# Performance work log

Measured on AMD Instinct MI355X. Metric: run time of the kernel, lower is better.

The kernel has to match this reference:

```python
import jax, jax.numpy as jnp
import numpy as np

D = 1024
H = 16
HD = D // H
T = 2048
B = 2
HID = 4 * D
EPS = 1e-5


def setup_inputs() -> dict:
    key = jax.random.key(0)
    ks = jax.random.split(key, 8)
    s = lambda fan_in: 1.0 / np.sqrt(fan_in)
    return {
        "x": jax.random.normal(ks[0], (B, T, D), dtype=jnp.float32),
        "ln1_g": jnp.ones((D,), jnp.float32),
        "ln1_b": jnp.zeros((D,), jnp.float32),
        "Wqkv": jax.random.uniform(ks[1], (D, 3 * D), jnp.float32, -s(D), s(D)),
        "bqkv": jnp.zeros((3 * D,), jnp.float32),
        "Wout": jax.random.uniform(ks[2], (D, D), jnp.float32, -s(D), s(D)),
        "bout": jnp.zeros((D,), jnp.float32),
        "ln2_g": jnp.ones((D,), jnp.float32),
        "ln2_b": jnp.zeros((D,), jnp.float32),
        "W1": jax.random.uniform(ks[3], (D, HID), jnp.float32, -s(D), s(D)),
        "b1": jnp.zeros((HID,), jnp.float32),
        "W2": jax.random.uniform(ks[4], (HID, D), jnp.float32, -s(HID), s(HID)),
        "b2": jnp.zeros((D,), jnp.float32),
    }


def _layernorm(h, g, b):
    mu = jnp.mean(h, axis=-1, keepdims=True)
    var = jnp.mean(jnp.square(h - mu), axis=-1, keepdims=True)
    return (h - mu) * jax.lax.rsqrt(var + EPS) * g + b


def reference(x, ln1_g, ln1_b, Wqkv, bqkv, Wout, bout, ln2_g, ln2_b, W1, b1, W2, b2):
    b, t, d = x.shape
    scale = 1.0 / np.sqrt(HD)

    # --- attention (pre-LN) ---
    h = _layernorm(x, ln1_g, ln1_b)
    qkv = h @ Wqkv + bqkv                      # [b, t, 3d]
    q, k, v = jnp.split(qkv, 3, axis=-1)
    q = q.reshape(b, t, H, HD)
    k = k.reshape(b, t, H, HD)
    v = v.reshape(b, t, H, HD)
    scores = jnp.einsum("bqhd,bkhd->bhqk", q, k) * scale  # [b, h, t, t]
    causal = jnp.tril(jnp.ones((t, t), dtype=bool))
    scores = jnp.where(causal, scores, -jnp.inf)
    attn = jax.nn.softmax(scores, axis=-1)
    out = jnp.einsum("bhqk,bkhd->bqhd", attn, v).reshape(b, t, d)
    x = x + (out @ Wout + bout)

    # --- MLP (pre-LN) ---
    h = _layernorm(x, ln2_g, ln2_b)
    h = jax.nn.gelu(h @ W1 + b1, approximate=False)
    x = x + (h @ W2 + b2)
    return x
```

## Files before the change

kernel.cpp:

```cpp
#include <hip/hip_runtime.h>
#include <hip/hip_bf16.h>
#include <math.h>

#define DD 1024
#define TT 2048
#define BB 2
#define HH 16
#define HDIM 64
#define HIDD 4096

typedef __attribute__((ext_vector_type(4))) float f32x4;
typedef __attribute__((ext_vector_type(8))) __bf16 bf16x8;
typedef __attribute__((ext_vector_type(4))) __bf16 bf16x4;

#define MF16 __builtin_amdgcn_mfma_f32_16x16x32_bf16

__device__ __forceinline__ void gload_lds16(const void* g, void* l) {
  __builtin_amdgcn_global_load_lds(
      (const __attribute__((address_space(1))) void*)g,
      (__attribute__((address_space(3))) void*)l, 16, 0, 0);
}

__global__ __launch_bounds__(256) void castT64(const float* __restrict__ W,
                                               __bf16* __restrict__ Wt,
                                               int K, int N) {
  __shared__ float t[64][65];
  const int n0 = blockIdx.x * 64, k0 = blockIdx.y * 64;
#pragma unroll
  for (int e = 0; e < 16; ++e) {
    int idx = e * 256 + threadIdx.x;
    int rr = idx >> 6, cc = idx & 63;
    t[rr][cc] = W[(size_t)(k0 + rr) * N + n0 + cc];
  }
  __syncthreads();
#pragma unroll
  for (int e = 0; e < 16; ++e) {
    int idx = e * 256 + threadIdx.x;
    int rr = idx >> 6, cc = idx & 63;
    Wt[(size_t)(n0 + rr) * K + k0 + cc] = (__bf16)t[cc][rr];
  }
}

__global__ __launch_bounds__(256) void ln_fwd(const float* __restrict__ x,
                                              const float* __restrict__ gamma,
                                              const float* __restrict__ beta,
                                              __bf16* __restrict__ out) {
  const int row = blockIdx.x;
  const int t4 = threadIdx.x;
  const float4 v = reinterpret_cast<const float4*>(x + (size_t)row * DD)[t4];
  float s = v.x + v.y + v.z + v.w;
  float ss = v.x * v.x + v.y * v.y + v.z * v.z + v.w * v.w;
#pragma unroll
  for (int m = 32; m >= 1; m >>= 1) { s += __shfl_xor(s, m); ss += __shfl_xor(ss, m); }
  __shared__ float red[8];
  const int wave = threadIdx.x >> 6, lane = threadIdx.x & 63;
  if (lane == 0) { red[wave] = s; red[4 + wave] = ss; }
  __syncthreads();
  s = red[0] + red[1] + red[2] + red[3];
  ss = red[4] + red[5] + red[6] + red[7];
  const float mu = s * (1.0f / DD);
  const float rs = rsqrtf(ss * (1.0f / DD) - mu * mu + 1e-5f);
  const float4 gm = reinterpret_cast<const float4*>(gamma)[t4];
  const float4 bt = reinterpret_cast<const float4*>(beta)[t4];
  bf16x4 o;
  o[0] = (__bf16)((v.x - mu) * rs * gm.x + bt.x);
  o[1] = (__bf16)((v.y - mu) * rs * gm.y + bt.y);
  o[2] = (__bf16)((v.z - mu) * rs * gm.z + bt.z);
  o[3] = (__bf16)((v.w - mu) * rs * gm.w + bt.w);
  *reinterpret_cast<bf16x4*>(out + (size_t)row * DD + t4 * 4) = o;
}

template <int MODE>
__global__ __launch_bounds__(512, 1) void gemm8(const __bf16* __restrict__ A,
                                                const __bf16* __restrict__ Bt,
                                                const float* __restrict__ bias,
                                                void* __restrict__ out0,
                                                __bf16* __restrict__ q1,
                                                __bf16* __restrict__ q2,
                                                __bf16* __restrict__ q3,
                                                int N, int K, int kchunk) {
  const int tid = threadIdx.x;
  const int wid = tid >> 6, lane = tid & 63;
  const int g = lane >> 4, r = lane & 15;
  const int wrh = wid >> 2;
  const int wc = (wid & 3) * 64;

  int bm, bn, kbase, zz;
  if constexpr (MODE == 3) {
    const int L = blockIdx.x;
    const int xcd = L & 7, idx = L >> 3;
    zz = xcd >> 1;
    bm = (((xcd & 1) << 3) + (idx >> 2)) * 256;
    bn = (idx & 3) * 256;
    kbase = zz * kchunk;
  } else {
    const int gx = gridDim.x;
    const int nwg = gx * gridDim.y;
    const int orig = blockIdx.y * gx + blockIdx.x;
    const int swz = (orig & 7) * (nwg >> 3) + (orig >> 3);
    const int bn4 = swz & 3;
    const int bmt = (swz >> 2) % gx;
    const int bng = (swz >> 2) / gx;
    bm = bmt * 256;
    bn = (bng * 4 + bn4) * 256;
    kbase = 0;
    zz = 0;
  }

  const int NT = kchunk >> 6;
  const __bf16* Asrc = A + (size_t)bm * K + kbase;
  const __bf16* Bsrc = Bt + (size_t)bn * K + kbase;

  __shared__ __bf16 lds[2][4][8192];

  f32x4 acc[8][4] = {};
  bf16x8 bfr[4][2];

  auto STG = [&](int ab, int h, int kt) {
    const __bf16* src = (ab ? Bsrc : Asrc) + (size_t)h * 128 * K;
    char* dst = (char*)&lds[kt & 1][ab * 2 + h][0];
#pragma unroll
    for (int gl = 0; gl < 2; ++gl) {
      const int o = gl * 8192 + wid * 1024 + lane * 16;
      const int row = o >> 7;
      const int cbs = (o & 127) ^ (((row >> 2) & 1) << 5);
      gload_lds16((const char*)src + (size_t)row * (K * 2) + kt * 128 + cbs,
                  dst + gl * 8192 + wid * 1024);
    }
  };
  auto DSA = [&](int s, int mi, int kk) -> bf16x8 {
    return *(const bf16x8*)((const char*)&lds[s][wrh][0] + (mi * 16 + r) * 128 +
                            ((kk * 64 + g * 16) ^ ((r & 4) << 3)));
  };
  auto DSB = [&](int s, int nj, int kk) -> bf16x8 {
    const int rt = wc + nj * 16 + r;
    return *(const bf16x8*)((const char*)&lds[s][2 + (rt >> 7)][0] + (rt & 127) * 128 +
                            ((kk * 64 + g * 16) ^ ((r & 4) << 3)));
  };

#define PH(S, Q, STAGE_STMT, WAIT_STMT)                                        \
  {                                                                            \
    if (Q == 0) {                                                              \
      _Pragma("unroll") for (int nj = 0; nj < 4; ++nj) {                       \
        bfr[nj][0] = DSB(S, nj, 0);                                            \
        bfr[nj][1] = DSB(S, nj, 1);                                            \
      }                                                                        \
    }                                                                          \
    bf16x8 a00 = DSA(S, 2 * Q, 0), a01 = DSA(S, 2 * Q, 1);                     \
    bf16x8 a10 = DSA(S, 2 * Q + 1, 0), a11 = DSA(S, 2 * Q + 1, 1);             \
    STAGE_STMT;                                                                \
    WAIT_STMT;                                                                 \
    __builtin_amdgcn_s_barrier();                                              \
    asm volatile("s_waitcnt lgkmcnt(0)" ::: "memory");                         \
    __builtin_amdgcn_s_setprio(1);                                             \
    _Pragma("unroll") for (int nj = 0; nj < 4; ++nj) {                         \
      acc[2 * Q][nj] = MF16(a00, bfr[nj][0], acc[2 * Q][nj], 0, 0, 0);         \
      acc[2 * Q][nj] = MF16(a01, bfr[nj][1], acc[2 * Q][nj], 0, 0, 0);         \
      acc[2 * Q + 1][nj] = MF16(a10, bfr[nj][0], acc[2 * Q + 1][nj], 0, 0, 0); \
      acc[2 * Q + 1][nj] = MF16(a11, bfr[nj][1], acc[2 * Q + 1][nj], 0, 0, 0); \
    }                                                                          \
    __builtin_amdgcn_s_setprio(0);                                             \
    __builtin_amdgcn_s_barrier();                                              \
  }

  STG(1, 0, 0); STG(1, 1, 0); STG(0, 0, 0); STG(0, 1, 0);
  STG(1, 0, 1); STG(1, 1, 1); STG(0, 0, 1);
  asm volatile("s_waitcnt vmcnt(6)" ::: "memory");
  __builtin_amdgcn_s_barrier();

  const int NI = NT >> 1;
  for (int i = 0; i < NI; ++i) {
    const int k2 = 2 * i + 2, k3 = 2 * i + 3;
    const bool nl = (i + 1 < NI);
    PH(0, 0, { STG(0, 1, 2 * i + 1); }, {});
    PH(0, 1, { if (nl) STG(1, 0, k2); }, {});
    PH(0, 2, { if (nl) STG(1, 1, k2); }, {});
    PH(0, 3, { if (nl) STG(0, 0, k2); },
       { if (nl) asm volatile("s_waitcnt vmcnt(6)" ::: "memory");
         else    asm volatile("s_waitcnt vmcnt(0)" ::: "memory"); });
    PH(1, 0, { if (nl) STG(0, 1, k2); }, {});
    PH(1, 1, { if (nl) STG(1, 0, k3); }, {});
    PH(1, 2, { if (nl) STG(1, 1, k3); }, {});
    PH(1, 3, { if (nl) STG(0, 0, k3); },
       { if (nl) asm volatile("s_waitcnt vmcnt(6)" ::: "memory"); });
  }
#undef PH

  const int row0 = bm + wrh * 128 + g * 4;
  const int col0 = bn + wc + r;
#pragma unroll
  for (int mi = 0; mi < 8; ++mi) {
#pragma unroll
    for (int nj = 0; nj < 4; ++nj) {
      const int col = col0 + nj * 16;
      float bv = 0.0f;
      if constexpr (MODE != 3) bv = bias[col];
#pragma unroll
      for (int i4 = 0; i4 < 4; ++i4) {
        const int rowg = row0 + mi * 16 + i4;
        const size_t idx = (size_t)rowg * N + col;
        const float v = acc[mi][nj][i4];
        if constexpr (MODE == 0) {
          if (bn >= 2048) {
            const int cv = col - 2048;
            const int hv = cv >> 6, dv = cv & 63;
            const int bq = rowg >> 11, tq = rowg & 2047;
            q1[(((size_t)bq * 16 + hv) * 64 + dv) * 2048 + tq] = (__bf16)(v + bv);
          } else {
            ((__bf16*)out0)[idx] = (__bf16)(v + bv);
          }
        } else if constexpr (MODE == 2) {
          const float t = v + bv;
          const float u2 = t * (1.5957691216f + t * t * 0.0713548163f);
          ((__bf16*)out0)[idx] = (__bf16)(t * __builtin_amdgcn_rcpf(1.0f + __expf(-u2)));
        } else {
          if (zz == 0) {
            ((float*)out0)[idx] = v;
          } else {
            __bf16* p = (zz == 1 ? q1 : (zz == 2 ? q2 : q3));
            p[idx] = (__bf16)v;
          }
        }
      }
    }
  }
}

__global__ __launch_bounds__(256) void reduceW2(const __bf16* __restrict__ p1,
                                                const __bf16* __restrict__ p2,
                                                const __bf16* __restrict__ p3,
                                                const float* __restrict__ x1,
                                                const float* __restrict__ b2,
                                                float* __restrict__ out) {
  const size_t i8 = ((size_t)blockIdx.x * 256 + threadIdx.x) * 8;
  const int col0 = (int)(i8 & 1023);
  bf16x8 a = *(const bf16x8*)(p1 + i8);
  bf16x8 b = *(const bf16x8*)(p2 + i8);
  bf16x8 c = *(const bf16x8*)(p3 + i8);
  float4 o0 = *(const float4*)(out + i8);
  float4 o1 = *(const float4*)(out + i8 + 4);
  const float4 xv0 = *(const float4*)(x1 + i8);
  const float4 xv1 = *(const float4*)(x1 + i8 + 4);
  const float4 bb0 = *(const float4*)(b2 + col0);
  const float4 bb1 = *(const float4*)(b2 + col0 + 4);
  float* op0 = (float*)&o0;
  float* op1 = (float*)&o1;
  const float* xp0 = (const float*)&xv0;
  const float* xp1 = (const float*)&xv1;
  const float* bp0 = (const float*)&bb0;
  const float* bp1 = (const float*)&bb1;
#pragma unroll
  for (int j = 0; j < 4; ++j)
    op0[j] += xp0[j] + bp0[j] + (float)a[j] + (float)b[j] + (float)c[j];
#pragma unroll
  for (int j = 0; j < 4; ++j)
    op1[j] += xp1[j] + bp1[j] + (float)a[4 + j] + (float)b[4 + j] + (float)c[4 + j];
  *(float4*)(out + i8) = o0;
  *(float4*)(out + i8 + 4) = o1;
}

template <int MODE>
__global__ __launch_bounds__(256) void gemm_bt(const __bf16* __restrict__ A,
                                               const __bf16* __restrict__ Bt,
                                               const float* __restrict__ bias,
                                               const float* __restrict__ resid,
                                               void* __restrict__ Cout,
                                               int M, int N, int K) {
  __shared__ __bf16 As[128 * 32];
  __shared__ __bf16 Bs[128 * 32];
  const int tid = threadIdx.x;
  const int wave = tid >> 6, lane = tid & 63;
  const int g = lane >> 4, r = lane & 15;
  const int gx = gridDim.x;
  const int nwg = gx * gridDim.y;
  const int orig = blockIdx.y * gx + blockIdx.x;
  const int swz = (orig & 7) * (nwg >> 3) + (orig >> 3);
  const int bn4 = swz & 3;
  const int bmt = (swz >> 2) % gx;
  const int bng = (swz >> 2) / gx;
  const int bm = bmt * 128;
  const int bn = (bng * 4 + bn4) * 128;
  const int wr = (wave >> 1) * 64, wc = (wave & 1) * 64;
  f32x4 acc[4][4] = {};

  const int off0 = wave * 2048 + lane * 16;
  const int off1 = off0 + 1024;
  const int sr0 = off0 >> 6, sk0 = (off0 & 63) >> 1;
  const int sr1 = off1 >> 6, sk1 = (off1 & 63) >> 1;
  const __bf16* gA0 = A + (size_t)(bm + sr0) * K + sk0;
  const __bf16* gA1 = A + (size_t)(bm + sr1) * K + sk1;
  const __bf16* gB0 = Bt + (size_t)(bn + sr0) * K + sk0;
  const __bf16* gB1 = Bt + (size_t)(bn + sr1) * K + sk1;
  char* lA0 = (char*)As + wave * 2048;
  char* lA1 = lA0 + 1024;
  char* lB0 = (char*)Bs + wave * 2048;
  char* lB1 = lB0 + 1024;

  for (int k0 = 0; k0 < K; k0 += 32) {
    gload_lds16(gA0 + k0, lA0);
    gload_lds16(gA1 + k0, lA1);
    gload_lds16(gB0 + k0, lB0);
    gload_lds16(gB1 + k0, lB1);
    __syncthreads();
    bf16x8 af[4], bf[4];
#pragma unroll
    for (int mi = 0; mi < 4; ++mi)
      af[mi] = *reinterpret_cast<const bf16x8*>(&As[(wr + mi * 16 + r) * 32 + g * 8]);
#pragma unroll
    for (int ni = 0; ni < 4; ++ni)
      bf[ni] = *reinterpret_cast<const bf16x8*>(&Bs[(wc + ni * 16 + r) * 32 + g * 8]);
    __builtin_amdgcn_s_setprio(1);
#pragma unroll
    for (int mi = 0; mi < 4; ++mi)
#pragma unroll
      for (int ni = 0; ni < 4; ++ni)
        acc[mi][ni] = MF16(af[mi], bf[ni], acc[mi][ni], 0, 0, 0);
    __builtin_amdgcn_s_setprio(0);
    __syncthreads();
  }

  const int row0 = bm + wr + 4 * g;
  const int col0 = bn + wc + r;
#pragma unroll
  for (int mi = 0; mi < 4; ++mi) {
#pragma unroll
    for (int ni = 0; ni < 4; ++ni) {
      const int col = col0 + ni * 16;
      const float bv = bias[col];
#pragma unroll
      for (int i = 0; i < 4; ++i) {
        const int row = row0 + mi * 16 + i;
        const size_t idx = (size_t)row * N + col;
        float v = acc[mi][ni][i] + bv;
        if (MODE == 0) {
          ((__bf16*)Cout)[idx] = (__bf16)v;
        } else if (MODE == 1) {
          ((float*)Cout)[idx] = v + resid[idx];
        } else {
          const float u2 = v * (1.5957691216f + v * v * 0.0713548163f);
          const float gl = v * __builtin_amdgcn_rcpf(1.0f + __expf(-u2));
          ((__bf16*)Cout)[idx] = (__bf16)gl;
        }
      }
    }
  }
}

__device__ __forceinline__ void stage_kv(const __bf16* __restrict__ src_row0, int rstride,
                                         int wave, int lane, char* tile) {
#pragma unroll
  for (int qq = 0; qq < 2; ++qq) {
    const int o = wave * 2048 + qq * 1024 + lane * 16;
    const int p = o >> 12, row = (o >> 6) & 63, cb = (o >> 4) & 3;
    gload_lds16(src_row0 + (size_t)row * rstride + p * 32 + cb * 8,
                tile + wave * 2048 + qq * 1024);
  }
}

__global__ __launch_bounds__(256) void attn_fwd(const __bf16* __restrict__ qkv,
                                                const __bf16* __restrict__ vtg,
                                                __bf16* __restrict__ atto) {
  const int orig = blockIdx.y * gridDim.x + blockIdx.x;
  const int swz = (orig & 7) * 64 + (orig >> 3);
  const int bh = swz >> 4;
  const int j = swz & 15;
  const int b = bh >> 4, h = bh & 15;
  const int tid = threadIdx.x;
  const int wave = tid >> 6, lane = tid & 63;
  const int g = lane >> 4, r = lane & 15;

  __shared__ __bf16 Qs[2 * 64 * 32];
  __shared__ __bf16 Ks[2][2 * 64 * 32];
  __shared__ __bf16 Vs[2][2 * 64 * 32];
  __shared__ __bf16 Pl[4][2 * 16 * 32];

  const __bf16* ksrc = qkv + (size_t)(b * TT) * 3072 + 1024 + h * 64;
  const __bf16* vsrc = vtg + (size_t)bh * 64 * 2048;
  const float C2 = 0.18033688011112042f;

  for (int ph = 0; ph < 2; ++ph) {
    const int qt = ph ? (31 - j) : j;
    const int q0 = qt * 64;
    stage_kv(qkv + (size_t)(b * TT + q0) * 3072 + h * 64, 3072, wave, lane, (char*)Qs);
    stage_kv(ksrc, 3072, wave, lane, (char*)Ks[0]);
    stage_kv(vsrc, 2048, wave, lane, (char*)Vs[0]);

    f32x4 oacc[4] = {};
    float m_s[4], l_s[4];
#pragma unroll
    for (int i = 0; i < 4; ++i) { m_s[i] = -1e30f; l_s[i] = 0.0f; }

    const int nt = qt + 1;
    int cur = 0;
    for (int t = 0; t < nt; ++t) {
      const int kv0 = t * 64;
      __syncthreads();
      if (t + 1 < nt) {
        stage_kv(ksrc + (size_t)(kv0 + 64) * 3072, 3072, wave, lane, (char*)Ks[cur ^ 1]);
        stage_kv(vsrc + kv0 + 64, 2048, wave, lane, (char*)Vs[cur ^ 1]);
      }
      bf16x8 qf[2];
#pragma unroll
      for (int kp = 0; kp < 2; ++kp)
        qf[kp] = *reinterpret_cast<const bf16x8*>(&Qs[kp * 2048 + (wave * 16 + r) * 32 + g * 8]);
      f32x4 s[4];
#pragma unroll
      for (int cn = 0; cn < 4; ++cn) s[cn] = f32x4{0.f, 0.f, 0.f, 0.f};
      __builtin_amdgcn_s_setprio(1);
#pragma unroll
      for (int cn = 0; cn < 4; ++cn)
#pragma unroll
        for (int kp = 0; kp < 2; ++kp) {
          bf16x8 bk = *reinterpret_cast<const bf16x8*>(
              &Ks[cur][kp * 2048 + (cn * 16 + r) * 32 + g * 8]);
          s[cn] = MF16(qf[kp], bk, s[cn], 0, 0, 0);
        }
      __builtin_amdgcn_s_setprio(0);
      const int rowg = q0 + wave * 16 + 4 * g;
      float pm[4];
#pragma unroll
      for (int i = 0; i < 4; ++i) pm[i] = -1e30f;
#pragma unroll
      for (int cn = 0; cn < 4; ++cn) {
        const int colg = kv0 + cn * 16 + r;
#pragma unroll
        for (int i = 0; i < 4; ++i) {
          float v = s[cn][i] * C2;
          v = (colg > rowg + i) ? -1e30f : v;
          s[cn][i] = v;
          pm[i] = fmaxf(pm[i], v);
        }
      }
      const int upd = __any((pm[0] > m_s[0] + 8.0f) || (pm[1] > m_s[1] + 8.0f) ||
                            (pm[2] > m_s[2] + 8.0f) || (pm[3] > m_s[3] + 8.0f));
      if (upd) {
#pragma unroll
        for (int i = 0; i < 4; ++i) {
          pm[i] = fmaxf(pm[i], __shfl_xor(pm[i], 1));
          pm[i] = fmaxf(pm[i], __shfl_xor(pm[i], 2));
          pm[i] = fmaxf(pm[i], __shfl_xor(pm[i], 4));
          pm[i] = fmaxf(pm[i], __shfl_xor(pm[i], 8));
          const float mn = fmaxf(m_s[i], pm[i]);
          const float sf = __builtin_amdgcn_exp2f(m_s[i] - mn);
          m_s[i] = mn;
          l_s[i] *= sf;
#pragma unroll
          for (int ni = 0; ni < 4; ++ni) oacc[ni][i] *= sf;
        }
      }
      float psum[4] = {0.f, 0.f, 0.f, 0.f};
#pragma unroll
      for (int cn = 0; cn < 4; ++cn)
#pragma unroll
        for (int i = 0; i < 4; ++i) {
          const float p = __builtin_amdgcn_exp2f(s[cn][i] - m_s[i]);
          s[cn][i] = p;
          psum[i] += p;
        }
#pragma unroll
      for (int i = 0; i < 4; ++i) {
        psum[i] += __shfl_xor(psum[i], 1);
        psum[i] += __shfl_xor(psum[i], 2);
        psum[i] += __shfl_xor(psum[i], 4);
        psum[i] += __shfl_xor(psum[i], 8);
        l_s[i] += psum[i];
      }
#pragma unroll
      for (int cn = 0; cn < 4; ++cn)
#pragma unroll
        for (int i = 0; i < 4; ++i)
          Pl[wave][(cn >> 1) * 512 + (4 * g + i) * 32 + (cn & 1) * 16 + r] = (__bf16)s[cn][i];
      bf16x8 pa[2];
#pragma unroll
      for (int kp = 0; kp < 2; ++kp)
        pa[kp] = *reinterpret_cast<const bf16x8*>(&Pl[wave][kp * 512 + r * 32 + g * 8]);
      __builtin_amdgcn_s_setprio(1);
#pragma unroll
      for (int ni = 0; ni < 4; ++ni)
#pragma unroll
        for (int kp = 0; kp < 2; ++kp) {
          bf16x8 bv = *reinterpret_cast<const bf16x8*>(
              &Vs[cur][kp * 2048 + (ni * 16 + r) * 32 + g * 8]);
          oacc[ni] = MF16(pa[kp], bv, oacc[ni], 0, 0, 0);
        }
      __builtin_amdgcn_s_setprio(0);
      cur ^= 1;
    }

#pragma unroll
    for (int i = 0; i < 4; ++i) {
      const float inv = 1.0f / l_s[i];
      const size_t rowo = (size_t)(b * TT + q0 + wave * 16 + 4 * g + i) * DD + h * 64;
#pragma unroll
      for (int ni = 0; ni < 4; ++ni)
        atto[rowo + ni * 16 + r] = (__bf16)(oacc[ni][i] * inv);
    }
    __syncthreads();
  }
}

extern "C" void kernel_launch(void* const* d_in, const int* in_sizes, int n_in,
                              void* d_out, int out_size, void* d_ws, size_t ws_size,
                              hipStream_t stream) {
  const float* x     = (const float*)d_in[0];
  const float* ln1_g = (const float*)d_in[1];
  const float* ln1_b = (const float*)d_in[2];
  const float* Wqkv  = (const float*)d_in[3];
  const float* bqkv  = (const float*)d_in[4];
  const float* Wout  = (const float*)d_in[5];
  const float* bout  = (const float*)d_in[6];
  const float* ln2_g = (const float*)d_in[7];
  const float* ln2_b = (const float*)d_in[8];
  const float* W1    = (const float*)d_in[9];
  const float* b1    = (const float*)d_in[10];
  const float* W2    = (const float*)d_in[11];
  const float* b2    = (const float*)d_in[12];
  float* out = (float*)d_out;

  char* ws = (char*)d_ws;
  const size_t MB = 1024 * 1024;
  __bf16* WqkvT = (__bf16*)(ws);
  __bf16* WoutT = (__bf16*)(ws + 6 * MB);
  __bf16* W1T   = (__bf16*)(ws + 8 * MB);
  __bf16* W2T   = (__bf16*)(ws + 16 * MB);
  float*  x1    = (float*)(ws + 24 * MB);
  __bf16* vtg   = (__bf16*)(ws + 24 * MB);
  __bf16* hbuf  = (__bf16*)(ws + 40 * MB);
  __bf16* qkvb  = (__bf16*)(ws + 48 * MB);
  __bf16* atto  = (__bf16*)(ws + 72 * MB);
  __bf16* mlp1  = (__bf16*)(ws + 48 * MB);
  __bf16* p1b   = (__bf16*)(ws);
  __bf16* p2b   = (__bf16*)(ws + 8 * MB);
  __bf16* p3b   = (__bf16*)(ws + 40 * MB);

  castT64<<<dim3(48, 16), 256, 0, stream>>>(Wqkv, WqkvT, 1024, 3072);
  castT64<<<dim3(16, 16), 256, 0, stream>>>(Wout, WoutT, 1024, 1024);
  castT64<<<dim3(64, 16), 256, 0, stream>>>(W1, W1T, 1024, 4096);
  castT64<<<dim3(16, 64), 256, 0, stream>>>(W2, W2T, 4096, 1024);

  ln_fwd<<<4096, 256, 0, stream>>>(x, ln1_g, ln1_b, hbuf);
  gemm8<0><<<dim3(16, 12), 512, 0, stream>>>(hbuf, WqkvT, bqkv, qkvb, vtg, nullptr, nullptr,
                                             3072, 1024, 1024);
  attn_fwd<<<dim3(16, 32), 256, 0, stream>>>(qkvb, vtg, atto);
  gemm_bt<1><<<dim3(32, 8), 256, 0, stream>>>(atto, WoutT, bout, x, x1, 4096, 1024, 1024);

  ln_fwd<<<4096, 256, 0, stream>>>(x1, ln2_g, ln2_b, hbuf);
  gemm8<2><<<dim3(16, 16), 512, 0, stream>>>(hbuf, W1T, b1, mlp1, nullptr, nullptr, nullptr,
                                             4096, 1024, 1024);
  gemm8<3><<<dim3(256, 1), 512, 0, stream>>>(mlp1, W2T, nullptr, out, p1b, p2b, p3b,
                                             1024, 4096, 1024);
  reduceW2<<<2048, 256, 0, stream>>>(p1b, p2b, p3b, x1, b2, out);
}
```

Baseline: 270.4 us.

## Move V transpose to a dedicated kernel and streamline attention softmax inner loop

The QKV GEMM epilogue no longer writes V transposed with scattered strided stores. A separate LDS-based transpose kernel now produces the V^T buffer with coalesced vector loads and stores. In attention, causal masking is skipped for tiles fully below the diagonal, and the per-iteration row-sum shuffle reduction is deferred to one reduction at the end. The P staging buffer in LDS also gets an XOR swizzle to reduce bank conflicts. The cost is an extra kernel launch and an additional read and write of V.

```diff
diff --git a/kernel.cpp b/kernel.cpp
--- a/kernel.cpp
+++ b/kernel.cpp
@@ -201,14 +201,7 @@
         const size_t idx = (size_t)rowg * N + col;
         const float v = acc[mi][nj][i4];
         if constexpr (MODE == 0) {
-          if (bn >= 2048) {
-            const int cv = col - 2048;
-            const int hv = cv >> 6, dv = cv & 63;
-            const int bq = rowg >> 11, tq = rowg & 2047;
-            q1[(((size_t)bq * 16 + hv) * 64 + dv) * 2048 + tq] = (__bf16)(v + bv);
-          } else {
-            ((__bf16*)out0)[idx] = (__bf16)(v + bv);
-          }
+          ((__bf16*)out0)[idx] = (__bf16)(v + bv);
         } else if constexpr (MODE == 2) {
           const float t = v + bv;
           const float u2 = t * (1.5957691216f + t * t * 0.0713548163f);
@@ -346,6 +339,37 @@
   }
 }
 
+__global__ __launch_bounds__(256) void vtrans(const __bf16* __restrict__ qkv,
+                                              __bf16* __restrict__ vtg) {
+  const int bh = blockIdx.y, b = bh >> 4, h = bh & 15;
+  const int t0 = blockIdx.x * 64;
+  const int tid = threadIdx.x, wave = tid >> 6, lane = tid & 63;
+  __shared__ __bf16 tile[64 * 64];
+#pragma unroll
+  for (int e = 0; e < 2; ++e) {
+    const int gid = e * 256 + tid;
+    const int row = gid >> 3, d0 = (gid & 7) * 8;
+    bf16x8 v = *reinterpret_cast<const bf16x8*>(
+        qkv + (size_t)(b * TT + t0 + row) * 3072 + 2048 + h * 64 + d0);
+    const int slot = (d0 >> 3) ^ (row & 7);
+    *reinterpret_cast<bf16x8*>((char*)tile + row * 128 + slot * 16) = v;
+  }
+  __syncthreads();
+  const int d = lane;
+#pragma unroll
+  for (int e = 0; e < 2; ++e) {
+    const int k0 = (wave * 2 + e) * 8;
+    bf16x8 o;
+#pragma unroll
+    for (int j = 0; j < 8; ++j) {
+      const int row = k0 + j;
+      o[j] = *(const __bf16*)((const char*)tile + row * 128 +
+                              (((d >> 3) ^ (row & 7)) << 4) + (d & 7) * 2);
+    }
+    *reinterpret_cast<bf16x8*>(&vtg[((size_t)bh * 64 + d) * 2048 + t0 + k0]) = o;
+  }
+}
+
 __device__ __forceinline__ void stage_kv(const __bf16* __restrict__ src_row0, int rstride,
                                          int wave, int lane, char* tile) {
 #pragma unroll
@@ -420,16 +444,27 @@
       float pm[4];
 #pragma unroll
       for (int i = 0; i < 4; ++i) pm[i] = -1e30f;
-#pragma unroll
-      for (int cn = 0; cn < 4; ++cn) {
-        const int colg = kv0 + cn * 16 + r;
-#pragma unroll
-        for (int i = 0; i < 4; ++i) {
-          float v = s[cn][i] * C2;
-          v = (colg > rowg + i) ? -1e30f : v;
-          s[cn][i] = v;
-          pm[i] = fmaxf(pm[i], v);
-        }
+      if (kv0 + 63 > q0 + wave * 16) {
+#pragma unroll
+        for (int cn = 0; cn < 4; ++cn) {
+          const int colg = kv0 + cn * 16 + r;
+#pragma unroll
+          for (int i = 0; i < 4; ++i) {
+            float v = s[cn][i] * C2;
+            v = (colg > rowg + i) ? -1e30f : v;
+            s[cn][i] = v;
+            pm[i] = fmaxf(pm[i], v);
+          }
+        }
+      } else {
+#pragma unroll
+        for (int cn = 0; cn < 4; ++cn)
+#pragma unroll
+          for (int i = 0; i < 4; ++i) {
+            const float v = s[cn][i] * C2;
+            s[cn][i] = v;
+            pm[i] = fmaxf(pm[i], v);
+          }
       }
       const int upd = __any((pm[0] > m_s[0] + 8.0f) || (pm[1] > m_s[1] + 8.0f) ||
                             (pm[2] > m_s[2] + 8.0f) || (pm[3] > m_s[3] + 8.0f));
@@ -448,32 +483,29 @@
           for (int ni = 0; ni < 4; ++ni) oacc[ni][i] *= sf;
         }
       }
-      float psum[4] = {0.f, 0.f, 0.f, 0.f};
 #pragma unroll
       for (int cn = 0; cn < 4; ++cn)
 #pragma unroll
         for (int i = 0; i < 4; ++i) {
           const float p = __builtin_amdgcn_exp2f(s[cn][i] - m_s[i]);
           s[cn][i] = p;
-          psum[i] += p;
-        }
-#pragma unroll
-      for (int i = 0; i < 4; ++i) {
-        psum[i] += __shfl_xor(psum[i], 1);
-        psum[i] += __shfl_xor(psum[i], 2);
-        psum[i] += __shfl_xor(psum[i], 4);
-        psum[i] += __shfl_xor(psum[i], 8);
-        l_s[i] += psum[i];
+          l_s[i] += p;
+        }
+#pragma unroll
+      for (int cn = 0; cn < 4; ++cn)
+#pragma unroll
+        for (int i = 0; i < 4; ++i) {
+          const int row = 4 * g + i;
+          const int byteoff = (cn >> 1) * 1024 +
+              ((row * 64 + (cn & 1) * 32 + r * 2) ^ ((row & 7) << 4));
+          *(__bf16*)((char*)&Pl[wave][0] + byteoff) = (__bf16)s[cn][i];
+        }
+      bf16x8 pa[2];
+#pragma unroll
+      for (int kp = 0; kp < 2; ++kp) {
+        const int byteoff = kp * 1024 + ((r * 64 + g * 16) ^ ((r & 7) << 4));
+        pa[kp] = *reinterpret_cast<const bf16x8*>((const char*)&Pl[wave][0] + byteoff);
       }
-#pragma unroll
-      for (int cn = 0; cn < 4; ++cn)
-#pragma unroll
-        for (int i = 0; i < 4; ++i)
-          Pl[wave][(cn >> 1) * 512 + (4 * g + i) * 32 + (cn & 1) * 16 + r] = (__bf16)s[cn][i];
-      bf16x8 pa[2];
-#pragma unroll
-      for (int kp = 0; kp < 2; ++kp)
-        pa[kp] = *reinterpret_cast<const bf16x8*>(&Pl[wave][kp * 512 + r * 32 + g * 8]);
       __builtin_amdgcn_s_setprio(1);
 #pragma unroll
       for (int ni = 0; ni < 4; ++ni)
@@ -489,7 +521,12 @@
 
 #pragma unroll
     for (int i = 0; i < 4; ++i) {
-      const float inv = 1.0f / l_s[i];
+      float l = l_s[i];
+      l += __shfl_xor(l, 1);
+      l += __shfl_xor(l, 2);
+      l += __shfl_xor(l, 4);
+      l += __shfl_xor(l, 8);
+      const float inv = 1.0f / l;
       const size_t rowo = (size_t)(b * TT + q0 + wave * 16 + 4 * g + i) * DD + h * 64;
 #pragma unroll
       for (int ni = 0; ni < 4; ++ni)
@@ -539,8 +576,9 @@
   castT64<<<dim3(16, 64), 256, 0, stream>>>(W2, W2T, 4096, 1024);
 
   ln_fwd<<<4096, 256, 0, stream>>>(x, ln1_g, ln1_b, hbuf);
-  gemm8<0><<<dim3(16, 12), 512, 0, stream>>>(hbuf, WqkvT, bqkv, qkvb, vtg, nullptr, nullptr,
+  gemm8<0><<<dim3(16, 12), 512, 0, stream>>>(hbuf, WqkvT, bqkv, qkvb, nullptr, nullptr, nullptr,
                                              3072, 1024, 1024);
+  vtrans<<<dim3(32, 32), 256, 0, stream>>>(qkvb, vtg);
   attn_fwd<<<dim3(16, 32), 256, 0, stream>>>(qkvb, vtg, atto);
   gemm_bt<1><<<dim3(32, 8), 256, 0, stream>>>(atto, WoutT, bout, x, x1, 4096, 1024, 1024);
 
```

New measurement: 240.9 us. -10.9%, faster.
